# Optimization experiments

Hardware: AMD Instinct MI355X
Metric: run time of the kernel (lower is better)

The kernel has to match this reference:

```python
import jax, jax.numpy as jnp
import numpy as np

B, N, F = 8, 1024, 256
OUT, REL = 256, 16
NADJ = 7  # ((2 relations + consecutive) * 2 for backward) + self link


def setup_inputs() -> dict:
    key = jax.random.key(0)
    k0, k1, k2, k3, k4 = jax.random.split(key, 5)
    features = jax.random.normal(k0, (B, N, F), dtype=jnp.float32)
    A1 = jax.random.uniform(k1, (B, N, N), dtype=jnp.float32)
    A2 = jax.random.uniform(k2, (B, N, N), dtype=jnp.float32)
    # learned params: one (F+REL, OUT) weight per adjacency matrix, edge embeddings init 'ones', bias (N, OUT)
    W = jax.random.normal(k3, (NADJ, F + REL, OUT), dtype=jnp.float32) * 0.05
    W_edges = jnp.ones((NADJ, REL), dtype=jnp.float32)
    b = jax.random.uniform(k4, (N, OUT), dtype=jnp.float32, minval=-0.05, maxval=0.05)
    return {"features": features, "A1": A1, "A2": A2, "W": W, "W_edges": W_edges, "b": b}


def reference(features, A1, A2, W, W_edges, b):
    # eye = A[0] * zeros(N) + eye(N)  -> batch-broadcast identity [B,N,N]
    eye = jnp.zeros_like(A1) + jnp.eye(N, dtype=A1.dtype)
    # original rolls along axis 0 (batch) of the broadcast identity (faithful replication)
    shifted = jnp.roll(eye, 1, axis=0)
    A_fwd = [A1, A2, shifted]                      # relations + consecutive link
    A_list = A_fwd + [jnp.swapaxes(a, 1, 2) for a in A_fwd]  # backward links
    A_list.append(eye)                             # self links
    A = jnp.stack(A_list, axis=0)                  # [R,B,N,N]

    # concat(features, tile(W_edges[r])) @ W[r] == features @ W[r][:F] + W_edges[r] @ W[r][F:]
    HW = jnp.einsum('bnf,rfo->rbno', features, W[:, :F]) \
         + jnp.einsum('rd,rdo->ro', W_edges, W[:, F:])[:, None, None, :]  # [R,B,N,OUT]
    AHW = jnp.einsum('rbnm,rbmo->rbno', A, HW)     # batched adjacency matmul
    out = jnp.max(AHW, axis=0) + b                 # max-aggregate over relations, add bias
    return out                                     # activation = linear
```

## Files before the change

### kernel.cpp

```cpp
#include <hip/hip_runtime.h>
#include <hip/hip_bf16.h>

#define B_ 8
#define N_ 1024
#define F_ 256
#define OUT_ 256
#define REL_ 16
#define NADJ_ 7

typedef __attribute__((ext_vector_type(8))) _Float16 f16x8;
typedef __attribute__((ext_vector_type(4))) float f32x4;

__device__ __forceinline__ void gll16(const _Float16* g, _Float16* l) {
    __builtin_amdgcn_global_load_lds(
        (const __attribute__((address_space(1))) void*)g,
        (__attribute__((address_space(3))) void*)l, 16, 0, 0);
}

__constant__ const int c_perm[7] = {0, 1, 3, 4, 2, 5, 6};

__global__ __launch_bounds__(256) void prep_kernel(const float* __restrict__ W,
                                                   const float* __restrict__ We,
                                                   const float* __restrict__ feat,
                                                   float* __restrict__ cb,
                                                   _Float16* __restrict__ WTp,
                                                   _Float16* __restrict__ Fe) {
    int bid = blockIdx.x, tid = threadIdx.x;
    if (bid < 7) {
        int idx = bid * 256 + tid;
        int j = idx / OUT_, o = idx % OUT_;
        int r = c_perm[j];
        const float* Wr = W + (size_t)r * (F_ + REL_) * OUT_;
        float s = 0.f;
#pragma unroll
        for (int d = 0; d < REL_; ++d) s += We[r * REL_ + d] * Wr[(F_ + d) * OUT_ + o];
        cb[idx] = s;
    } else if (bid < 1799) {
        int idx = (bid - 7) * 256 + tid;
        int j = idx >> 16, rem = idx & 65535, o = rem >> 8, f = rem & 255;
        int r = c_perm[j];
        WTp[idx] = (_Float16)W[((size_t)r * (F_ + REL_) + f) * OUT_ + o];
    } else {
        int i = (bid - 1799) * 256 + tid;
        size_t base = (size_t)i * 8;
        float4 a = *(const float4*)(feat + base);
        float4 b = *(const float4*)(feat + base + 4);
        f16x8 v = {(_Float16)a.x, (_Float16)a.y, (_Float16)a.z, (_Float16)a.w,
                   (_Float16)b.x, (_Float16)b.y, (_Float16)b.z, (_Float16)b.w};
        *(f16x8*)(Fe + base) = v;
    }
}

__global__ __launch_bounds__(256) void convhw_kernel(const float* __restrict__ A1,
                                                     const float* __restrict__ A2,
                                                     const _Float16* __restrict__ Fe,
                                                     const _Float16* __restrict__ WTp,
                                                     const float* __restrict__ cb,
                                                     _Float16* __restrict__ Af,
                                                     _Float16* __restrict__ HWT,
                                                     _Float16* __restrict__ HWN) {
    __shared__ _Float16 S[8192];
    const int bid = blockIdx.x, tid = threadIdx.x;
    if (bid < 896) {
        const int z = bid / 128, rem = bid % 128, bx = rem & 63, by = rem >> 6;
        const bool tr = (z < 4);
        const _Float16* A  = tr ? (WTp + (size_t)z * 65536) : Fe;
        const _Float16* Bt = tr ? Fe : (WTp + (size_t)z * 65536);
        const int m0 = (tr ? by : bx) * 128;
        const int n0 = (tr ? bx : by) * 128;
        _Float16* As = S;
        _Float16* Bs = S + 4096;
        const int wave = tid >> 6, lane = tid & 63, lm = lane & 15, q = lane >> 4;
        const int wr = (wave >> 1) * 64, wc = (wave & 1) * 64;
        const int srow = tid >> 2, sk = (tid & 3) * 8;
        const _Float16* ga0 = A + (size_t)(m0 + srow) * F_ + sk;
        const _Float16* ga1 = ga0 + (size_t)64 * F_;
        const _Float16* gb0 = Bt + (size_t)(n0 + srow) * F_ + sk;
        const _Float16* gb1 = gb0 + (size_t)64 * F_;
        _Float16* la0 = As + tid * 8;
        _Float16* la1 = As + 2048 + tid * 8;
        _Float16* lb0 = Bs + tid * 8;
        _Float16* lb1 = Bs + 2048 + tid * 8;

        f32x4 acc[4][4] = {};
        for (int k0 = 0; k0 < F_; k0 += 32) {
            gll16(ga0 + k0, la0);
            gll16(ga1 + k0, la1);
            gll16(gb0 + k0, lb0);
            gll16(gb1 + k0, lb1);
            __syncthreads();
            f16x8 af[4], bf[4];
#pragma unroll
            for (int i = 0; i < 4; ++i) af[i] = *(const f16x8*)(As + (wr + i * 16 + lm) * 32 + q * 8);
#pragma unroll
            for (int j = 0; j < 4; ++j) bf[j] = *(const f16x8*)(Bs + (wc + j * 16 + lm) * 32 + q * 8);
#pragma unroll
            for (int i = 0; i < 4; ++i)
#pragma unroll
                for (int j = 0; j < 4; ++j)
                    acc[i][j] = __builtin_amdgcn_mfma_f32_16x16x32_f16(af[i], bf[j], acc[i][j], 0, 0, 0);
            __syncthreads();
        }
        const float* cbz = cb + (size_t)z * 256;
        if (tr) {
            _Float16* C = HWT + (size_t)z * ((size_t)256 * 8192);
#pragma unroll
            for (int i = 0; i < 4; ++i)
#pragma unroll
                for (int j = 0; j < 4; ++j)
#pragma unroll
                    for (int g = 0; g < 4; ++g) {
                        int row = wr + i * 16 + q * 4 + g;
                        int col = wc + j * 16 + lm;
                        float v = acc[i][j][g] + cbz[m0 + row];
                        C[(size_t)(m0 + row) * 8192 + (n0 + col)] = (_Float16)v;
                    }
        } else {
            _Float16* C = HWN + (size_t)(z - 4) * ((size_t)8192 * 256);
#pragma unroll
            for (int i = 0; i < 4; ++i)
#pragma unroll
                for (int j = 0; j < 4; ++j)
#pragma unroll
                    for (int g = 0; g < 4; ++g) {
                        int row = wr + i * 16 + q * 4 + g;
                        int col = wc + j * 16 + lm;
                        float v = acc[i][j][g] + cbz[n0 + col];
                        C[(size_t)(m0 + row) * 256 + (n0 + col)] = (_Float16)v;
                    }
        }
    } else {
        _Float16* T = S;
        const int cbid = bid - 896;
        int z = cbid >> 8, s = z >> 3, b = z & 7;
        const float* src = (s ? A2 : A1) + (size_t)b * N_ * N_;
        int k0 = (cbid & 15) * 64, n0 = ((cbid >> 4) & 15) * 64;
        int r = tid >> 2, cs = (tid & 3) * 16;
        const float* sp = src + (size_t)(k0 + r) * N_ + n0 + cs;
        _Float16 v[16];
#pragma unroll
        for (int j = 0; j < 16; j += 4) {
            float4 f = *(const float4*)(sp + j);
            v[j] = (_Float16)f.x; v[j + 1] = (_Float16)f.y;
            v[j + 2] = (_Float16)f.z; v[j + 3] = (_Float16)f.w;
        }
        const size_t slab = (size_t)8 * N_ * N_;
#pragma unroll
        for (int j = 0; j < 16; ++j) {
            int n = cs + j;
            int sw = ((n ^ (n >> 3)) & 7) << 3;
            T[n * 64 + (r ^ sw)] = v[j];
        }
        __syncthreads();
        {
            int n = tid >> 2, i2 = (tid & 3) * 16;
            int sw = ((n ^ (n >> 3)) & 7) << 3;
            f16x8 q0 = *(const f16x8*)&T[n * 64 + (i2 ^ sw)];
            f16x8 q1 = *(const f16x8*)&T[n * 64 + ((i2 + 8) ^ sw)];
            _Float16* dt = Af + (size_t)s * slab + (size_t)b * N_ * N_ + (size_t)(n0 + n) * N_ + k0 + i2;
            *(f16x8*)dt = q0;
            *(f16x8*)(dt + 8) = q1;
        }
    }
}

__global__ __launch_bounds__(256) void p2_kernel(const float* __restrict__ A1,
                                                 const float* __restrict__ A2,
                                                 const _Float16* __restrict__ Af,
                                                 const _Float16* __restrict__ HWT,
                                                 _Float16* __restrict__ AHW) {
    __shared__ _Float16 As[128 * 32];
    __shared__ _Float16 Bs[128 * 32];
    const int d = blockIdx.x;
    const int member = (d >> 3) & 1;
    const int p = (d & 7) | ((d >> 4) << 3);
    const int mt = p & 7, zz = p >> 3;
    const int rr = zz >> 3, b = zz & 7;
    const _Float16* Bt = HWT + (size_t)rr * (256 * 8192) + (size_t)b * 1024;
    _Float16* C = AHW + (size_t)rr * (8 * 262144) + (size_t)b * 262144;
    const int m0 = mt * 128, n0 = member * 128;
    const int tid = threadIdx.x;
    const int wave = tid >> 6, lane = tid & 63, lm = lane & 15, q = lane >> 4;
    const int wr = (wave >> 1) * 64, wc = (wave & 1) * 64;
    const int srow = tid >> 2, sk = (tid & 3) * 8;
    const _Float16* gb0 = Bt + (size_t)(n0 + srow) * 8192 + sk;
    const _Float16* gb1 = gb0 + (size_t)64 * 8192;
    _Float16* la0 = As + tid * 8;
    _Float16* la1 = As + 2048 + tid * 8;
    _Float16* lb0 = Bs + tid * 8;
    _Float16* lb1 = Bs + 2048 + tid * 8;

    f32x4 acc[4][4] = {};
    if (rr < 2) {
        const float* Ag0 = ((rr & 1) ? A2 : A1) + (size_t)b * N_ * N_
                           + (size_t)(m0 + srow) * N_ + sk;
        const float* Ag1 = Ag0 + (size_t)64 * N_;
        float4 pa0 = *(const float4*)(Ag0);
        float4 pa1 = *(const float4*)(Ag0 + 4);
        float4 pb0 = *(const float4*)(Ag1);
        float4 pb1 = *(const float4*)(Ag1 + 4);
        for (int k0 = 0; k0 < N_; k0 += 32) {
            f16x8 v0 = {(_Float16)pa0.x, (_Float16)pa0.y, (_Float16)pa0.z, (_Float16)pa0.w,
                        (_Float16)pa1.x, (_Float16)pa1.y, (_Float16)pa1.z, (_Float16)pa1.w};
            f16x8 v1 = {(_Float16)pb0.x, (_Float16)pb0.y, (_Float16)pb0.z, (_Float16)pb0.w,
                        (_Float16)pb1.x, (_Float16)pb1.y, (_Float16)pb1.z, (_Float16)pb1.w};
            *(f16x8*)la0 = v0;
            *(f16x8*)la1 = v1;
            gll16(gb0 + k0, lb0);
            gll16(gb1 + k0, lb1);
            if (k0 + 32 < N_) {
                pa0 = *(const float4*)(Ag0 + k0 + 32);
                pa1 = *(const float4*)(Ag0 + k0 + 36);
                pb0 = *(const float4*)(Ag1 + k0 + 32);
                pb1 = *(const float4*)(Ag1 + k0 + 36);
            }
            __syncthreads();
            f16x8 af[4], bf[4];
#pragma unroll
            for (int i = 0; i < 4; ++i) af[i] = *(const f16x8*)(As + (wr + i * 16 + lm) * 32 + q * 8);
#pragma unroll
            for (int j = 0; j < 4; ++j) bf[j] = *(const f16x8*)(Bs + (wc + j * 16 + lm) * 32 + q * 8);
#pragma unroll
            for (int i = 0; i < 4; ++i)
#pragma unroll
                for (int j = 0; j < 4; ++j)
                    acc[i][j] = __builtin_amdgcn_mfma_f32_16x16x32_f16(af[i], bf[j], acc[i][j], 0, 0, 0);
            __syncthreads();
        }
    } else {
        const _Float16* ga0 = Af + (size_t)(rr - 2) * (8 * 1048576) + (size_t)b * 1048576
                              + (size_t)(m0 + srow) * N_ + sk;
        const _Float16* ga1 = ga0 + (size_t)64 * N_;
        for (int k0 = 0; k0 < N_; k0 += 32) {
            gll16(ga0 + k0, la0);
            gll16(ga1 + k0, la1);
            gll16(gb0 + k0, lb0);
            gll16(gb1 + k0, lb1);
            __syncthreads();
            f16x8 af[4], bf[4];
#pragma unroll
            for (int i = 0; i < 4; ++i) af[i] = *(const f16x8*)(As + (wr + i * 16 + lm) * 32 + q * 8);
#pragma unroll
            for (int j = 0; j < 4; ++j) bf[j] = *(const f16x8*)(Bs + (wc + j * 16 + lm) * 32 + q * 8);
#pragma unroll
            for (int i = 0; i < 4; ++i)
#pragma unroll
                for (int j = 0; j < 4; ++j)
                    acc[i][j] = __builtin_amdgcn_mfma_f32_16x16x32_f16(af[i], bf[j], acc[i][j], 0, 0, 0);
            __syncthreads();
        }
    }
#pragma unroll
    for (int i = 0; i < 4; ++i)
#pragma unroll
        for (int j = 0; j < 4; ++j)
#pragma unroll
            for (int g = 0; g < 4; ++g) {
                int row = wr + i * 16 + q * 4 + g;
                int col = wc + j * 16 + lm;
                C[(size_t)(m0 + row) * 256 + (n0 + col)] = (_Float16)acc[i][j][g];
            }
}

__global__ __launch_bounds__(256) void max_kernel(const _Float16* __restrict__ AHW,
                                                  const _Float16* __restrict__ HWN,
                                                  const float* __restrict__ bias,
                                                  float* __restrict__ out) {
    size_t i = ((size_t)blockIdx.x * 256 + threadIdx.x) * 8;
    const size_t slab = (size_t)B_ * N_ * OUT_;
    float m[8];
    f16x8 v = *(const f16x8*)(AHW + i);
#pragma unroll
    for (int e = 0; e < 8; ++e) m[e] = (float)v[e];
#pragma unroll
    for (int rr = 1; rr < 4; ++rr) {
        f16x8 w = *(const f16x8*)(AHW + rr * slab + i);
#pragma unroll
        for (int e = 0; e < 8; ++e) m[e] = fmaxf(m[e], (float)w[e]);
    }
#pragma unroll
    for (int j = 0; j < 3; ++j) {
        f16x8 w = *(const f16x8*)(HWN + j * slab + i);
#pragma unroll
        for (int e = 0; e < 8; ++e) m[e] = fmaxf(m[e], (float)w[e]);
    }
    size_t bidx = i & ((size_t)N_ * OUT_ - 1);
    float4 b0 = *(const float4*)(bias + bidx);
    float4 b1 = *(const float4*)(bias + bidx + 4);
    float4 o0 = {m[0] + b0.x, m[1] + b0.y, m[2] + b0.z, m[3] + b0.w};
    float4 o1 = {m[4] + b1.x, m[5] + b1.y, m[6] + b1.z, m[7] + b1.w};
    *(float4*)(out + i) = o0;
    *(float4*)(out + i + 4) = o1;
}

__global__ void cbias_kernel(const float* __restrict__ W, const float* __restrict__ We,
                             float* __restrict__ c) {
    int idx = blockIdx.x * 256 + threadIdx.x;
    if (idx >= NADJ_ * OUT_) return;
    int r = idx / OUT_, o = idx % OUT_;
    const float* Wr = W + (size_t)r * (F_ + REL_) * OUT_;
    float s = 0.f;
#pragma unroll
    for (int d = 0; d < REL_; ++d) s += We[r * REL_ + d] * Wr[(F_ + d) * OUT_ + o];
    c[idx] = s;
}

__global__ __launch_bounds__(256) void hw_kernel(const float* __restrict__ feat,
                                                 const float* __restrict__ W,
                                                 const float* __restrict__ cb,
                                                 _Float16* __restrict__ HWb) {
    __shared__ _Float16 As[64][32];
    __shared__ _Float16 Bs[64][32];
    const int mt = blockIdx.x, ct = blockIdx.y;
    const int tid = threadIdx.x, wave = tid >> 6, lane = tid & 63;
    const int r = (ct * 64) / OUT_;
    const int o0 = (ct * 64) % OUT_;
    const float* Bg = W + (size_t)r * (F_ + REL_) * OUT_ + o0;
    const int m0 = mt * 64;
    const int lm = lane & 15, q = lane >> 4;
    f32x4 acc[4] = {};
    for (int k0 = 0; k0 < F_; k0 += 32) {
        {
            int seg = (tid & 3) * 8, m = tid >> 2;
            const float* src = feat + (size_t)(m0 + m) * F_ + k0 + seg;
#pragma unroll
            for (int j = 0; j < 8; ++j) As[m][seg + j] = (_Float16)src[j];
        }
        {
            int kk = tid >> 3, ns = (tid & 7) * 8;
            const float* src = Bg + (size_t)(k0 + kk) * OUT_ + ns;
#pragma unroll
            for (int j = 0; j < 8; ++j) Bs[ns + j][kk] = (_Float16)src[j];
        }
        __syncthreads();
        f16x8 a = *(const f16x8*)&As[wave * 16 + lm][q * 8];
#pragma unroll
        for (int c4 = 0; c4 < 4; ++c4) {
            f16x8 b = *(const f16x8*)&Bs[c4 * 16 + lm][q * 8];
            acc[c4] = __builtin_amdgcn_mfma_f32_16x16x32_f16(a, b, acc[c4], 0, 0, 0);
        }
        __syncthreads();
    }
#pragma unroll
    for (int c4 = 0; c4 < 4; ++c4)
#pragma unroll
        for (int g = 0; g < 4; ++g) {
            int row = wave * 16 + (lane >> 4) * 4 + g;
            int col = c4 * 16 + lm;
            float v = acc[c4][g] + cb[r * OUT_ + o0 + col];
            HWb[((size_t)r * B_ * N_ + m0 + row) * OUT_ + o0 + col] = (_Float16)v;
        }
}

__global__ __launch_bounds__(256) void agg_kernel(const float* __restrict__ A1,
                                                  const float* __restrict__ A2,
                                                  const _Float16* __restrict__ HWb,
                                                  const float* __restrict__ bias,
                                                  float* __restrict__ out) {
    __shared__ _Float16 As[64][32];
    __shared__ _Float16 Bs[64][32];
    const int b = blockIdx.z, nt = blockIdx.y, ot = blockIdx.x;
    const int tid = threadIdx.x, wave = tid >> 6, lane = tid & 63;
    const int n0 = nt * 64, o0 = ot * 64;
    const int lm = lane & 15, q = lane >> 4;
    const size_t rstride = (size_t)B_ * N_ * OUT_;
    f32x4 mx[4];
#pragma unroll
    for (int i = 0; i < 4; ++i) mx[i] = f32x4{-1e30f, -1e30f, -1e30f, -1e30f};
#pragma unroll 1
    for (int rr = 0; rr < 4; ++rr) {
        const float* Ag = ((rr & 1) ? A2 : A1) + (size_t)b * N_ * N_;
        const bool tr = (rr >= 2);
        const int r = (rr < 2) ? rr : rr + 1;
        const _Float16* Bg = HWb + (size_t)r * rstride + (size_t)b * N_ * OUT_ + o0;
        f32x4 acc[4] = {};
        for (int k0 = 0; k0 < N_; k0 += 32) {
            if (!tr) {
                int seg = (tid & 3) * 8, m = tid >> 2;
                const float* src = Ag + (size_t)(n0 + m) * N_ + k0 + seg;
#pragma unroll
                for (int j = 0; j < 8; ++j) As[m][seg + j] = (_Float16)src[j];
            } else {
                int kk = tid >> 3, ms = (tid & 7) * 8;
                const float* src = Ag + (size_t)(k0 + kk) * N_ + n0 + ms;
#pragma unroll
                for (int j = 0; j < 8; ++j) As[ms + j][kk] = (_Float16)src[j];
            }
            {
                int kk = tid >> 3, ns = (tid & 7) * 8;
                const _Float16* src = Bg + (size_t)(k0 + kk) * OUT_ + ns;
#pragma unroll
                for (int j = 0; j < 8; ++j) Bs[ns + j][kk] = src[j];
            }
            __syncthreads();
            f16x8 a = *(const f16x8*)&As[wave * 16 + lm][q * 8];
#pragma unroll
            for (int c4 = 0; c4 < 4; ++c4) {
                f16x8 bb = *(const f16x8*)&Bs[c4 * 16 + lm][q * 8];
                acc[c4] = __builtin_amdgcn_mfma_f32_16x16x32_f16(a, bb, acc[c4], 0, 0, 0);
            }
            __syncthreads();
        }
#pragma unroll
        for (int c4 = 0; c4 < 4; ++c4)
#pragma unroll
            for (int g = 0; g < 4; ++g) mx[c4][g] = fmaxf(mx[c4][g], acc[c4][g]);
    }
#pragma unroll
    for (int c4 = 0; c4 < 4; ++c4)
#pragma unroll
        for (int g = 0; g < 4; ++g) {
            int row = wave * 16 + (lane >> 4) * 4 + g;
            int col = c4 * 16 + lm;
            size_t pos = ((size_t)b * N_ + n0 + row) * OUT_ + o0 + col;
            float v = mx[c4][g];
            v = fmaxf(v, (float)HWb[2 * rstride + pos]);
            v = fmaxf(v, (float)HWb[5 * rstride + pos]);
            v = fmaxf(v, (float)HWb[6 * rstride + pos]);
            out[pos] = v + bias[((size_t)(n0 + row)) * OUT_ + o0 + col];
        }
}

extern "C" void kernel_launch(void* const* d_in, const int* in_sizes, int n_in,
                              void* d_out, int out_size, void* d_ws, size_t ws_size,
                              hipStream_t stream) {
    const float* feat = (const float*)d_in[0];
    const float* A1   = (const float*)d_in[1];
    const float* A2   = (const float*)d_in[2];
    const float* W    = (const float*)d_in[3];
    const float* We   = (const float*)d_in[4];
    const float* bias = (const float*)d_in[5];
    float* out = (float*)d_out;

    const size_t OFF_CB   = 0;
    const size_t OFF_WT   = 8192;
    const size_t OFF_FE   = 1048576;
    const size_t OFF_AF   = 5242880;
    const size_t OFF_HWT  = 72351744;
    const size_t OFF_HWN  = 89128960;
    const size_t OFF_AHW  = 101711872;
    const size_t WS_NEEDED = 118489088;

    if (ws_size >= WS_NEEDED) {
        float*    cbp = (float*)((char*)d_ws + OFF_CB);
        _Float16* WTp = (_Float16*)((char*)d_ws + OFF_WT);
        _Float16* Fe  = (_Float16*)((char*)d_ws + OFF_FE);
        _Float16* Af  = (_Float16*)((char*)d_ws + OFF_AF);
        _Float16* HWT = (_Float16*)((char*)d_ws + OFF_HWT);
        _Float16* HWN = (_Float16*)((char*)d_ws + OFF_HWN);
        _Float16* AHW = (_Float16*)((char*)d_ws + OFF_AHW);

        prep_kernel<<<2823, 256, 0, stream>>>(W, We, feat, cbp, WTp, Fe);
        convhw_kernel<<<4992, 256, 0, stream>>>(A1, A2, Fe, WTp, cbp, Af, HWT, HWN);
        p2_kernel<<<512, 256, 0, stream>>>(A1, A2, Af, HWT, AHW);
        max_kernel<<<1024, 256, 0, stream>>>(AHW, HWN, bias, out);
    } else {
        float* cb = (float*)d_ws;
        _Float16* HWb = (_Float16*)((char*)d_ws + 8192);
        cbias_kernel<<<7, 256, 0, stream>>>(W, We, cb);
        hw_kernel<<<dim3(128, 28), 256, 0, stream>>>(feat, W, cb, HWb);
        agg_kernel<<<dim3(4, 16, 8), 256, 0, stream>>>(A1, A2, HWb, bias, out);
    }
}
```

Before: 178.7 us.

## Fuse adjacency transpose and fp16 conversion into p2 GEMM loads, drop Af buffer

Removes the separate pass that transposed A1/A2 into a half-precision Af workspace. The transposed-relation branch of p2_kernel now reads fp32 A columns directly, converts them in registers and writes them into LDS already transposed, with a register prefetch of the next k-slab. An XOR swizzle on the A tile in LDS is added to both branches to reduce bank conflicts. This saves a 64MB write and read of Af and one kernel's worth of blocks, at the cost of scalar fp16x2 LDS stores and fp32 global reads inside the GEMM loop.

```diff
diff --git a/kernel.cpp b/kernel.cpp
--- a/kernel.cpp
+++ b/kernel.cpp
@@ -9,6 +9,7 @@
 #define NADJ_ 7
 
 typedef __attribute__((ext_vector_type(8))) _Float16 f16x8;
+typedef __attribute__((ext_vector_type(2))) _Float16 f16x2;
 typedef __attribute__((ext_vector_type(4))) float f32x4;
 
 __device__ __forceinline__ void gll16(const _Float16* g, _Float16* l) {
@@ -51,122 +52,84 @@
     }
 }
 
-__global__ __launch_bounds__(256) void convhw_kernel(const float* __restrict__ A1,
-                                                     const float* __restrict__ A2,
-                                                     const _Float16* __restrict__ Fe,
-                                                     const _Float16* __restrict__ WTp,
-                                                     const float* __restrict__ cb,
-                                                     _Float16* __restrict__ Af,
-                                                     _Float16* __restrict__ HWT,
-                                                     _Float16* __restrict__ HWN) {
+__global__ __launch_bounds__(256) void hw7_kernel(const _Float16* __restrict__ Fe,
+                                                  const _Float16* __restrict__ WTp,
+                                                  const float* __restrict__ cb,
+                                                  _Float16* __restrict__ HWT,
+                                                  _Float16* __restrict__ HWN) {
     __shared__ _Float16 S[8192];
     const int bid = blockIdx.x, tid = threadIdx.x;
-    if (bid < 896) {
-        const int z = bid / 128, rem = bid % 128, bx = rem & 63, by = rem >> 6;
-        const bool tr = (z < 4);
-        const _Float16* A  = tr ? (WTp + (size_t)z * 65536) : Fe;
-        const _Float16* Bt = tr ? Fe : (WTp + (size_t)z * 65536);
-        const int m0 = (tr ? by : bx) * 128;
-        const int n0 = (tr ? bx : by) * 128;
-        _Float16* As = S;
-        _Float16* Bs = S + 4096;
-        const int wave = tid >> 6, lane = tid & 63, lm = lane & 15, q = lane >> 4;
-        const int wr = (wave >> 1) * 64, wc = (wave & 1) * 64;
-        const int srow = tid >> 2, sk = (tid & 3) * 8;
-        const _Float16* ga0 = A + (size_t)(m0 + srow) * F_ + sk;
-        const _Float16* ga1 = ga0 + (size_t)64 * F_;
-        const _Float16* gb0 = Bt + (size_t)(n0 + srow) * F_ + sk;
-        const _Float16* gb1 = gb0 + (size_t)64 * F_;
-        _Float16* la0 = As + tid * 8;
-        _Float16* la1 = As + 2048 + tid * 8;
-        _Float16* lb0 = Bs + tid * 8;
-        _Float16* lb1 = Bs + 2048 + tid * 8;
-
-        f32x4 acc[4][4] = {};
-        for (int k0 = 0; k0 < F_; k0 += 32) {
-            gll16(ga0 + k0, la0);
-            gll16(ga1 + k0, la1);
-            gll16(gb0 + k0, lb0);
-            gll16(gb1 + k0, lb1);
-            __syncthreads();
-            f16x8 af[4], bf[4];
-#pragma unroll
-            for (int i = 0; i < 4; ++i) af[i] = *(const f16x8*)(As + (wr + i * 16 + lm) * 32 + q * 8);
-#pragma unroll
-            for (int j = 0; j < 4; ++j) bf[j] = *(const f16x8*)(Bs + (wc + j * 16 + lm) * 32 + q * 8);
-#pragma unroll
-            for (int i = 0; i < 4; ++i)
-#pragma unroll
-                for (int j = 0; j < 4; ++j)
-                    acc[i][j] = __builtin_amdgcn_mfma_f32_16x16x32_f16(af[i], bf[j], acc[i][j], 0, 0, 0);
-            __syncthreads();
-        }
-        const float* cbz = cb + (size_t)z * 256;
-        if (tr) {
-            _Float16* C = HWT + (size_t)z * ((size_t)256 * 8192);
-#pragma unroll
-            for (int i = 0; i < 4; ++i)
-#pragma unroll
-                for (int j = 0; j < 4; ++j)
-#pragma unroll
-                    for (int g = 0; g < 4; ++g) {
-                        int row = wr + i * 16 + q * 4 + g;
-                        int col = wc + j * 16 + lm;
-                        float v = acc[i][j][g] + cbz[m0 + row];
-                        C[(size_t)(m0 + row) * 8192 + (n0 + col)] = (_Float16)v;
-                    }
-        } else {
-            _Float16* C = HWN + (size_t)(z - 4) * ((size_t)8192 * 256);
-#pragma unroll
-            for (int i = 0; i < 4; ++i)
-#pragma unroll
-                for (int j = 0; j < 4; ++j)
-#pragma unroll
-                    for (int g = 0; g < 4; ++g) {
-                        int row = wr + i * 16 + q * 4 + g;
-                        int col = wc + j * 16 + lm;
-                        float v = acc[i][j][g] + cbz[n0 + col];
-                        C[(size_t)(m0 + row) * 256 + (n0 + col)] = (_Float16)v;
-                    }
-        }
+    const int z = bid / 128, rem = bid % 128, bx = rem & 63, by = rem >> 6;
+    const bool tr = (z < 4);
+    const _Float16* A  = tr ? (WTp + (size_t)z * 65536) : Fe;
+    const _Float16* Bt = tr ? Fe : (WTp + (size_t)z * 65536);
+    const int m0 = (tr ? by : bx) * 128;
+    const int n0 = (tr ? bx : by) * 128;
+    _Float16* As = S;
+    _Float16* Bs = S + 4096;
+    const int wave = tid >> 6, lane = tid & 63, lm = lane & 15, q = lane >> 4;
+    const int wr = (wave >> 1) * 64, wc = (wave & 1) * 64;
+    const int srow = tid >> 2, sk = (tid & 3) * 8;
+    const _Float16* ga0 = A + (size_t)(m0 + srow) * F_ + sk;
+    const _Float16* ga1 = ga0 + (size_t)64 * F_;
+    const _Float16* gb0 = Bt + (size_t)(n0 + srow) * F_ + sk;
+    const _Float16* gb1 = gb0 + (size_t)64 * F_;
+    _Float16* la0 = As + tid * 8;
+    _Float16* la1 = As + 2048 + tid * 8;
+    _Float16* lb0 = Bs + tid * 8;
+    _Float16* lb1 = Bs + 2048 + tid * 8;
+
+    f32x4 acc[4][4] = {};
+    for (int k0 = 0; k0 < F_; k0 += 32) {
+        gll16(ga0 + k0, la0);
+        gll16(ga1 + k0, la1);
+        gll16(gb0 + k0, lb0);
+        gll16(gb1 + k0, lb1);
+        __syncthreads();
+        f16x8 af[4], bf[4];
+#pragma unroll
+        for (int i = 0; i < 4; ++i) af[i] = *(const f16x8*)(As + (wr + i * 16 + lm) * 32 + q * 8);
+#pragma unroll
+        for (int j = 0; j < 4; ++j) bf[j] = *(const f16x8*)(Bs + (wc + j * 16 + lm) * 32 + q * 8);
+#pragma unroll
+        for (int i = 0; i < 4; ++i)
+#pragma unroll
+            for (int j = 0; j < 4; ++j)
+                acc[i][j] = __builtin_amdgcn_mfma_f32_16x16x32_f16(af[i], bf[j], acc[i][j], 0, 0, 0);
+        __syncthreads();
+    }
+    const float* cbz = cb + (size_t)z * 256;
+    if (tr) {
+        _Float16* C = HWT + (size_t)z * ((size_t)256 * 8192);
+#pragma unroll
+        for (int i = 0; i < 4; ++i)
+#pragma unroll
+            for (int j = 0; j < 4; ++j)
+#pragma unroll
+                for (int g = 0; g < 4; ++g) {
+                    int row = wr + i * 16 + q * 4 + g;
+                    int col = wc + j * 16 + lm;
+                    float v = acc[i][j][g] + cbz[m0 + row];
+                    C[(size_t)(m0 + row) * 8192 + (n0 + col)] = (_Float16)v;
+                }
     } else {
-        _Float16* T = S;
-        const int cbid = bid - 896;
-        int z = cbid >> 8, s = z >> 3, b = z & 7;
-        const float* src = (s ? A2 : A1) + (size_t)b * N_ * N_;
-        int k0 = (cbid & 15) * 64, n0 = ((cbid >> 4) & 15) * 64;
-        int r = tid >> 2, cs = (tid & 3) * 16;
-        const float* sp = src + (size_t)(k0 + r) * N_ + n0 + cs;
-        _Float16 v[16];
-#pragma unroll
-        for (int j = 0; j < 16; j += 4) {
-            float4 f = *(const float4*)(sp + j);
-            v[j] = (_Float16)f.x; v[j + 1] = (_Float16)f.y;
-            v[j + 2] = (_Float16)f.z; v[j + 3] = (_Float16)f.w;
-        }
-        const size_t slab = (size_t)8 * N_ * N_;
-#pragma unroll
-        for (int j = 0; j < 16; ++j) {
-            int n = cs + j;
-            int sw = ((n ^ (n >> 3)) & 7) << 3;
-            T[n * 64 + (r ^ sw)] = v[j];
-        }
-        __syncthreads();
-        {
-            int n = tid >> 2, i2 = (tid & 3) * 16;
-            int sw = ((n ^ (n >> 3)) & 7) << 3;
-            f16x8 q0 = *(const f16x8*)&T[n * 64 + (i2 ^ sw)];
-            f16x8 q1 = *(const f16x8*)&T[n * 64 + ((i2 + 8) ^ sw)];
-            _Float16* dt = Af + (size_t)s * slab + (size_t)b * N_ * N_ + (size_t)(n0 + n) * N_ + k0 + i2;
-            *(f16x8*)dt = q0;
-            *(f16x8*)(dt + 8) = q1;
-        }
+        _Float16* C = HWN + (size_t)(z - 4) * ((size_t)8192 * 256);
+#pragma unroll
+        for (int i = 0; i < 4; ++i)
+#pragma unroll
+            for (int j = 0; j < 4; ++j)
+#pragma unroll
+                for (int g = 0; g < 4; ++g) {
+                    int row = wr + i * 16 + q * 4 + g;
+                    int col = wc + j * 16 + lm;
+                    float v = acc[i][j][g] + cbz[n0 + col];
+                    C[(size_t)(m0 + row) * 256 + (n0 + col)] = (_Float16)v;
+                }
     }
 }
 
 __global__ __launch_bounds__(256) void p2_kernel(const float* __restrict__ A1,
                                                  const float* __restrict__ A2,
-                                                 const _Float16* __restrict__ Af,
                                                  const _Float16* __restrict__ HWT,
                                                  _Float16* __restrict__ AHW) {
     __shared__ _Float16 As[128 * 32];
@@ -185,15 +148,16 @@
     const int srow = tid >> 2, sk = (tid & 3) * 8;
     const _Float16* gb0 = Bt + (size_t)(n0 + srow) * 8192 + sk;
     const _Float16* gb1 = gb0 + (size_t)64 * 8192;
-    _Float16* la0 = As + tid * 8;
-    _Float16* la1 = As + 2048 + tid * 8;
     _Float16* lb0 = Bs + tid * 8;
     _Float16* lb1 = Bs + 2048 + tid * 8;
-
+    const int swv = (tid >> 6) & 3;
+    _Float16* la0 = As + (tid >> 2) * 32 + (((tid & 3) ^ swv) * 8);
+    _Float16* la1 = la0 + 2048;
+
+    const float* Ag = ((rr & 1) ? A2 : A1) + (size_t)b * N_ * N_;
     f32x4 acc[4][4] = {};
     if (rr < 2) {
-        const float* Ag0 = ((rr & 1) ? A2 : A1) + (size_t)b * N_ * N_
-                           + (size_t)(m0 + srow) * N_ + sk;
+        const float* Ag0 = Ag + (size_t)(m0 + srow) * N_ + sk;
         const float* Ag1 = Ag0 + (size_t)64 * N_;
         float4 pa0 = *(const float4*)(Ag0);
         float4 pa1 = *(const float4*)(Ag0 + 4);
@@ -217,9 +181,11 @@
             __syncthreads();
             f16x8 af[4], bf[4];
 #pragma unroll
-            for (int i = 0; i < 4; ++i) af[i] = *(const f16x8*)(As + (wr + i * 16 + lm) * 32 + q * 8);
-#pragma unroll
-            for (int j = 0; j < 4; ++j) bf[j] = *(const f16x8*)(Bs + (wc + j * 16 + lm) * 32 + q * 8);
+            for (int i = 0; i < 4; ++i)
+                af[i] = *(const f16x8*)(As + (wr + i * 16 + lm) * 32 + ((q ^ i) * 8));
+#pragma unroll
+            for (int j = 0; j < 4; ++j)
+                bf[j] = *(const f16x8*)(Bs + (wc + j * 16 + lm) * 32 + q * 8);
 #pragma unroll
             for (int i = 0; i < 4; ++i)
 #pragma unroll
@@ -228,20 +194,41 @@
             __syncthreads();
         }
     } else {
-        const _Float16* ga0 = Af + (size_t)(rr - 2) * (8 * 1048576) + (size_t)b * 1048576
-                              + (size_t)(m0 + srow) * N_ + sk;
-        const _Float16* ga1 = ga0 + (size_t)64 * N_;
+        const int kk = (tid >> 4) * 2, ms = (tid & 15) * 8;
+        const int sw = (ms >> 4) & 3;
+        _Float16* wp = As + ms * 32 + (kk ^ (sw << 3));
+        const float* ga = Ag + (size_t)kk * N_ + m0 + ms;
+        float4 pa0 = *(const float4*)(ga);
+        float4 pa1 = *(const float4*)(ga + 4);
+        float4 pb0 = *(const float4*)(ga + N_);
+        float4 pb1 = *(const float4*)(ga + N_ + 4);
         for (int k0 = 0; k0 < N_; k0 += 32) {
-            gll16(ga0 + k0, la0);
-            gll16(ga1 + k0, la1);
+            f16x2 w;
+            w = f16x2{(_Float16)pa0.x, (_Float16)pb0.x}; *(f16x2*)(wp + 0 * 32) = w;
+            w = f16x2{(_Float16)pa0.y, (_Float16)pb0.y}; *(f16x2*)(wp + 1 * 32) = w;
+            w = f16x2{(_Float16)pa0.z, (_Float16)pb0.z}; *(f16x2*)(wp + 2 * 32) = w;
+            w = f16x2{(_Float16)pa0.w, (_Float16)pb0.w}; *(f16x2*)(wp + 3 * 32) = w;
+            w = f16x2{(_Float16)pa1.x, (_Float16)pb1.x}; *(f16x2*)(wp + 4 * 32) = w;
+            w = f16x2{(_Float16)pa1.y, (_Float16)pb1.y}; *(f16x2*)(wp + 5 * 32) = w;
+            w = f16x2{(_Float16)pa1.z, (_Float16)pb1.z}; *(f16x2*)(wp + 6 * 32) = w;
+            w = f16x2{(_Float16)pa1.w, (_Float16)pb1.w}; *(f16x2*)(wp + 7 * 32) = w;
             gll16(gb0 + k0, lb0);
             gll16(gb1 + k0, lb1);
+            if (k0 + 32 < N_) {
+                ga += (size_t)32 * N_;
+                pa0 = *(const float4*)(ga);
+                pa1 = *(const float4*)(ga + 4);
+                pb0 = *(const float4*)(ga + N_);
+                pb1 = *(const float4*)(ga + N_ + 4);
+            }
             __syncthreads();
             f16x8 af[4], bf[4];
 #pragma unroll
-            for (int i = 0; i < 4; ++i) af[i] = *(const f16x8*)(As + (wr + i * 16 + lm) * 32 + q * 8);
-#pragma unroll
-            for (int j = 0; j < 4; ++j) bf[j] = *(const f16x8*)(Bs + (wc + j * 16 + lm) * 32 + q * 8);
+            for (int i = 0; i < 4; ++i)
+                af[i] = *(const f16x8*)(As + (wr + i * 16 + lm) * 32 + ((q ^ i) * 8));
+#pragma unroll
+            for (int j = 0; j < 4; ++j)
+                bf[j] = *(const f16x8*)(Bs + (wc + j * 16 + lm) * 32 + q * 8);
 #pragma unroll
             for (int i = 0; i < 4; ++i)
 #pragma unroll
@@ -435,24 +422,22 @@
     const size_t OFF_CB   = 0;
     const size_t OFF_WT   = 8192;
     const size_t OFF_FE   = 1048576;
-    const size_t OFF_AF   = 5242880;
-    const size_t OFF_HWT  = 72351744;
-    const size_t OFF_HWN  = 89128960;
-    const size_t OFF_AHW  = 101711872;
-    const size_t WS_NEEDED = 118489088;
+    const size_t OFF_HWT  = 5242880;
+    const size_t OFF_HWN  = 22020096;
+    const size_t OFF_AHW  = 34603008;
+    const size_t WS_NEEDED = 51380224;
 
     if (ws_size >= WS_NEEDED) {
         float*    cbp = (float*)((char*)d_ws + OFF_CB);
         _Float16* WTp = (_Float16*)((char*)d_ws + OFF_WT);
         _Float16* Fe  = (_Float16*)((char*)d_ws + OFF_FE);
-        _Float16* Af  = (_Float16*)((char*)d_ws + OFF_AF);
         _Float16* HWT = (_Float16*)((char*)d_ws + OFF_HWT);
         _Float16* HWN = (_Float16*)((char*)d_ws + OFF_HWN);
         _Float16* AHW = (_Float16*)((char*)d_ws + OFF_AHW);
 
         prep_kernel<<<2823, 256, 0, stream>>>(W, We, feat, cbp, WTp, Fe);
-        convhw_kernel<<<4992, 256, 0, stream>>>(A1, A2, Fe, WTp, cbp, Af, HWT, HWN);
-        p2_kernel<<<512, 256, 0, stream>>>(A1, A2, Af, HWT, AHW);
+        hw7_kernel<<<896, 256, 0, stream>>>(Fe, WTp, cbp, HWT, HWN);
+        p2_kernel<<<512, 256, 0, stream>>>(A1, A2, HWT, AHW);
         max_kernel<<<1024, 256, 0, stream>>>(AHW, HWN, bias, out);
     } else {
         float* cb = (float*)d_ws;
```

After: 188.7 us. +5.6%, slower.
